# Kernel optimization log

Hardware: AMD Instinct MI355X
Metric: run time of the kernel (lower is better)

## Reference

```python
import jax, jax.numpy as jnp
import numpy as np

PAD_CODE = -1
COMMIT_WEIGHT = 0.25

B, N, D, K = 16, 4096, 256, 512


def setup_inputs() -> dict:
    key = jax.random.key(0)
    k1, k2, k3 = jax.random.split(key, 3)
    z = jax.random.normal(k1, (B, N, D), dtype=jnp.float32)
    phoneme_mask = jax.random.uniform(k2, (B, N)) > 0.3
    codebook = jax.random.normal(k3, (K, D), dtype=jnp.float32)
    return {"z": z, "phoneme_mask": phoneme_mask, "codebook": codebook}


def reference(z, phoneme_mask, codebook):
    # Nearest-codebook search: ||z - e||^2 = ||z||^2 - 2 z.e + ||e||^2
    z_sq = jnp.sum(z * z, axis=-1, keepdims=True)                # (B, N, 1)
    e_sq = jnp.sum(codebook * codebook, axis=-1)                 # (K,)
    cross = jnp.einsum("bnd,kd->bnk", z, codebook)              # (B, N, K)
    dists = z_sq - 2.0 * cross + e_sq                            # (B, N, K)
    indices = jnp.argmin(dists, axis=-1)                         # (B, N) int

    embed = codebook[indices]                                    # gather (B, N, D)
    # straight-through estimator: forward = embed, backward passes grad to z
    quantized = z + jax.lax.stop_gradient(embed - z)
    # commitment loss (quantize detached, as in lucidrains VectorQuantize)
    commit_loss = COMMIT_WEIGHT * jnp.mean(
        (jax.lax.stop_gradient(quantized) - z) ** 2
    )

    # mask padded positions
    indices = jnp.where(phoneme_mask, indices, jnp.full_like(indices, PAD_CODE))
    quantized = quantized * phoneme_mask[..., None].astype(quantized.dtype)
    return quantized, indices, commit_loss
```

## Files before the change

kernel.cpp:

```cpp
#include <hip/hip_runtime.h>

#define BN    65536
#define DD    256
#define KCB   512
#define MT    256
#define NBLK  256
#define NST   16

typedef __attribute__((ext_vector_type(8))) short bf16x8;
typedef __attribute__((ext_vector_type(4))) float f32x4;

static __device__ __forceinline__ float bf2f(unsigned short u) {
  return __uint_as_float(((unsigned int)u) << 16);
}
static __device__ __forceinline__ unsigned short f2bf(float f) {
  unsigned int u = __float_as_uint(f);
  return (unsigned short)((u + 0x7fffu + ((u >> 16) & 1u)) >> 16);
}
static __device__ __forceinline__ void gll16(const void* g, void* l) {
  __builtin_amdgcn_global_load_lds(
      (const __attribute__((address_space(1))) unsigned int*)g,
      (__attribute__((address_space(3))) unsigned int*)l, 16, 0, 0);
}

__global__ void vq_zero_ws(float* ws) { ws[0] = 0.f; }

__global__ void vq_prep(const float* __restrict__ cbg,
                        char* __restrict__ cbt,
                        float* __restrict__ esq) {
  const int tid = threadIdx.x, lane = tid & 63, wave = tid >> 6;
  const int code = blockIdx.x * 4 + wave;
  float4 v = ((const float4*)cbg)[(size_t)code * 64 + lane];
  ushort4 h, l;
  h.x = f2bf(v.x); l.x = f2bf(v.x - bf2f(h.x));
  h.y = f2bf(v.y); l.y = f2bf(v.y - bf2f(h.y));
  h.z = f2bf(v.z); l.z = f2bf(v.z - bf2f(h.z));
  h.w = f2bf(v.w); l.w = f2bf(v.w - bf2f(h.w));
  const int s  = code >> 5;
  const int lc = code & 31;
  unsigned raw = (unsigned)(lc * 512 + lane * 8);
  unsigned off = (unsigned)(s * 32768) + (raw ^ ((unsigned)(lc & 7) << 4));
  *(ushort4*)(cbt + off)         = h;
  *(ushort4*)(cbt + off + 16384) = l;
  double sq = (double)v.x * v.x + (double)v.y * v.y +
              (double)v.z * v.z + (double)v.w * v.w;
#pragma unroll
  for (int m = 1; m < 64; m <<= 1) sq += __shfl_xor(sq, m, 64);
  if (lane == 0) esq[code] = (float)sq;
}

#define ISSUE(S, BSEL)                                                       \
  do {                                                                       \
    const char* _src = cbt + (size_t)(S) * 32768 + (size_t)tid * 16;         \
    char* _dst = &bufB[BSEL][tid * 16];                                      \
    _Pragma("unroll")                                                        \
    for (int _r = 0; _r < 4; ++_r)                                           \
      gll16(_src + _r * 8192, _dst + _r * 8192);                             \
  } while (0)

#define VMCNT4 asm volatile("s_waitcnt vmcnt(4)" ::: "memory")
#define VMCNT0 asm volatile("s_waitcnt vmcnt(0)" ::: "memory")
#define SBAR   asm volatile("s_barrier" ::: "memory")

__global__ __launch_bounds__(512, 2) void vq_main(
    const float* __restrict__ zg,
    const int* __restrict__ maskg,
    const float* __restrict__ cbg,
    const char* __restrict__ cbt,
    const float* __restrict__ esqg,
    float* __restrict__ outq,
    float* __restrict__ outidx,
    float* __restrict__ wsum)
{
  __shared__ __align__(16) char bufB[2][32768];
  __shared__ float esqs[KCB];
  __shared__ float zsqs[MT];
  __shared__ float v1s[MT], v2s[MT];
  __shared__ int   i1s[MT];
  __shared__ float carr[MT];
  __shared__ int   fidxs[MT], maskb[MT], flaglist[MT];
  __shared__ int   flagcnt, mflags;
  __shared__ double rbd[8];
  __shared__ int    rbi[8];

  const int tid   = threadIdx.x;
  const int lane  = tid & 63;
  const int wave  = tid >> 6;
  const int q     = lane >> 4;
  const int l15   = lane & 15;
  const int m0    = blockIdx.x * MT;
  const int rbase = wave * 32;

  if (tid == 0) { flagcnt = 0; mflags = 0; }

  int wm = 0;
  if (tid < 128) {
    unsigned int W = ((const unsigned int*)maskg)[tid];
    if (W > 1u) wm |= 1;
    if (W != 0u && W != 0x3f800000u) wm |= 2;
    unsigned int lo = W & 0xffffu, hi = W >> 16;
    if ((lo != 0u && lo != 0x3f80u) || (hi != 0u && hi != 0x3f80u)) wm |= 4;
  }
  if (wm) atomicOr(&mflags, wm);

  esqs[tid] = esqg[tid];

  ISSUE(0, 0);

  bf16x8 ah[2][8], al[2][8];
  float zacc0 = 0.f, zacc1 = 0.f;
#pragma unroll
  for (int i = 0; i < 2; ++i) {
    const int grow = m0 + rbase + i * 16 + l15;
#pragma unroll
    for (int kk = 0; kk < 8; ++kk) {
      const float* src = &zg[(size_t)grow * DD + kk * 32 + q * 8];
      float4 v0 = *(const float4*)src;
      float4 v1 = *(const float4*)(src + 4);
      float f[8] = {v0.x, v0.y, v0.z, v0.w, v1.x, v1.y, v1.z, v1.w};
      union { ushort us[8]; bf16x8 v; } H, L;
#pragma unroll
      for (int e = 0; e < 8; ++e) {
        unsigned short hh = f2bf(f[e]);
        H.us[e] = hh;
        L.us[e] = f2bf(f[e] - bf2f(hh));
      }
      ah[i][kk] = H.v;
      al[i][kk] = L.v;
      float s = 0.f;
#pragma unroll
      for (int e = 0; e < 8; ++e) s = fmaf(f[e], f[e], s);
      if (i == 0) zacc0 += s; else zacc1 += s;
    }
  }
  {
    float s0 = zacc0, s1 = zacc1;
    s0 += __shfl_xor(s0, 16, 64); s0 += __shfl_xor(s0, 32, 64);
    s1 += __shfl_xor(s1, 16, 64); s1 += __shfl_xor(s1, 32, 64);
    if (q == 0) {
      zsqs[rbase + l15]      = s0;
      zsqs[rbase + 16 + l15] = s1;
    }
  }
  __syncthreads();
  const int mmode = mflags;

  float t1[2][4], t2[2][4];
  int   ti[2][4];
#pragma unroll
  for (int i = 0; i < 2; ++i)
#pragma unroll
    for (int rr = 0; rr < 4; ++rr) { t1[i][rr] = 3.0e38f; t2[i][rr] = 3.0e38f; ti[i][rr] = 0; }

#pragma unroll 1
  for (int s = 0; s < NST; ++s) {
    if (s < NST - 1) { ISSUE(s + 1, (s + 1) & 1); VMCNT4; }
    else             { VMCNT0; }
    SBAR;
    const char* bb = &bufB[s & 1][0];
#pragma unroll
    for (int tt = 0; tt < 2; ++tt) {
      const int lc = tt * 16 + l15;
      const unsigned sw = ((unsigned)(lc & 7)) << 4;
      f32x4 a0 = (f32x4){0.f, 0.f, 0.f, 0.f};
      f32x4 a1 = (f32x4){0.f, 0.f, 0.f, 0.f};
#pragma unroll
      for (int kk = 0; kk < 8; ++kk) {
        const unsigned off = ((unsigned)(lc * 512 + kk * 64 + q * 16)) ^ sw;
        bf16x8 bh = *(const bf16x8*)(bb + off);
        bf16x8 bl = *(const bf16x8*)(bb + 16384 + off);
        a0 = __builtin_amdgcn_mfma_f32_16x16x32_bf16(ah[0][kk], bh, a0, 0, 0, 0);
        a1 = __builtin_amdgcn_mfma_f32_16x16x32_bf16(ah[1][kk], bh, a1, 0, 0, 0);
        a0 = __builtin_amdgcn_mfma_f32_16x16x32_bf16(al[0][kk], bh, a0, 0, 0, 0);
        a1 = __builtin_amdgcn_mfma_f32_16x16x32_bf16(al[1][kk], bh, a1, 0, 0, 0);
        a0 = __builtin_amdgcn_mfma_f32_16x16x32_bf16(ah[0][kk], bl, a0, 0, 0, 0);
        a1 = __builtin_amdgcn_mfma_f32_16x16x32_bf16(ah[1][kk], bl, a1, 0, 0, 0);
      }
      const int code = s * 32 + lc;
      const float eh = 0.5f * esqs[code];
#pragma unroll
      for (int rr = 0; rr < 4; ++rr) {
        {
          float v = eh - a0[rr];
          bool  tk = v < t1[0][rr];
          float m2 = fminf(t2[0][rr], v);
          t2[0][rr] = tk ? t1[0][rr] : m2;
          ti[0][rr] = tk ? code : ti[0][rr];
          t1[0][rr] = tk ? v : t1[0][rr];
        }
        {
          float v = eh - a1[rr];
          bool  tk = v < t1[1][rr];
          float m2 = fminf(t2[1][rr], v);
          t2[1][rr] = tk ? t1[1][rr] : m2;
          ti[1][rr] = tk ? code : ti[1][rr];
          t1[1][rr] = tk ? v : t1[1][rr];
        }
      }
    }
    SBAR;
  }

#pragma unroll
  for (int i = 0; i < 2; ++i)
#pragma unroll
    for (int rr = 0; rr < 4; ++rr) {
      float a1 = t1[i][rr], a2 = t2[i][rr];
      int   ai = ti[i][rr];
#pragma unroll
      for (int m = 1; m < 16; m <<= 1) {
        float o1 = __shfl_xor(a1, m, 64);
        float o2 = __shfl_xor(a2, m, 64);
        int   oi = __shfl_xor(ai, m, 64);
        bool  tk = (o1 < a1) || (o1 == a1 && oi < ai);
        float losr = tk ? a1 : o1;
        a2 = fminf(fminf(a2, o2), losr);
        a1 = tk ? o1 : a1;
        ai = tk ? oi : ai;
      }
      if (l15 == 0) {
        int row = rbase + i * 16 + q * 4 + rr;
        v1s[row] = a1; v2s[row] = a2; i1s[row] = ai;
      }
    }
  __syncthreads();

  if (tid < MT) {
    float bv1 = v1s[tid], bv2 = v2s[tid];
    int   bi = i1s[tid];
    fidxs[tid] = bi;
    carr[tid]  = zsqs[tid] + 2.f * bv1;
    if (2.f * (bv2 - bv1) < 0.02f) {
      int pos = atomicAdd(&flagcnt, 1);
      flaglist[pos] = tid;
    }
    int mk;
    if (!(mmode & 1))      mk = maskg[m0 + tid] ? 1 : 0;
    else if (!(mmode & 2)) mk = ((const float*)maskg)[m0 + tid] != 0.f ? 1 : 0;
    else if (!(mmode & 4)) mk = ((const unsigned short*)maskg)[m0 + tid] ? 1 : 0;
    else                   mk = ((const unsigned char*)maskg)[m0 + tid] ? 1 : 0;
    maskb[tid] = mk;
  }
  __syncthreads();

  int nflag = flagcnt;
  for (int f = 0; f < nflag; ++f) {
    int row = flaglist[f];
    int k   = tid;
    double d2 = 0.0;
    for (int d = 0; d < DD; ++d) {
      double df = (double)zg[(size_t)(m0 + row) * DD + d] - (double)cbg[(size_t)k * DD + d];
      d2 = fma(df, df, d2);
    }
    double bd = d2;
    int    bk = k;
    for (int m = 1; m < 64; m <<= 1) {
      double od = __shfl_xor(bd, m, 64);
      int    ok = __shfl_xor(bk, m, 64);
      if (od < bd || (od == bd && ok < bk)) { bd = od; bk = ok; }
    }
    if (lane == 0) { rbd[wave] = bd; rbi[wave] = bk; }
    __syncthreads();
    if (tid == 0) {
      double xd = rbd[0]; int xk = rbi[0];
      for (int w = 1; w < 8; ++w)
        if (rbd[w] < xd || (rbd[w] == xd && rbi[w] < xk)) { xd = rbd[w]; xk = rbi[w]; }
      fidxs[row] = xk;
      carr[row]  = (float)xd;
    }
    __syncthreads();
  }
  __syncthreads();

  if (tid < MT)
    outidx[m0 + tid] = maskb[tid] ? (float)(fidxs[tid] & (KCB - 1)) : -1.0f;

  if (tid < MT) {
    float c = carr[tid];
    for (int m = 1; m < 64; m <<= 1) c += __shfl_xor(c, m, 64);
    if (lane == 0) atomicAdd(wsum, c);
  }

#pragma unroll
  for (int it = 0; it < 32; ++it) {
    int idx = it * 512 + tid;
    int row = idx >> 6;
    int f4  = idx & 63;
    int k   = fidxs[row] & (KCB - 1);
    float4 val = {0.f, 0.f, 0.f, 0.f};
    if (maskb[row]) val = ((const float4*)cbg)[(size_t)k * 64 + f4];
    ((float4*)outq)[(size_t)(m0 + row) * 64 + f4] = val;
  }
}

__global__ __launch_bounds__(256, 3) void vq_main_fb(
    const float* __restrict__ zg, const int* __restrict__ maskg,
    const float* __restrict__ cbg, float* __restrict__ outq,
    float* __restrict__ outidx, float* __restrict__ wsum)
{
  __shared__ unsigned short zs_hi[8 * 32 * 32];
  __shared__ unsigned short zs_lo[8 * 32 * 32];
  __shared__ float esqs[KCB];
  __shared__ float zsq[32];
  __shared__ float wv1[4][32], wv2[4][32];
  __shared__ int   wi1[4][32];
  __shared__ float carr[32];
  __shared__ int   fidxs[32], maskb[32], flaglist[32];
  __shared__ int   flagcnt, mflags;
  __shared__ double rbd[4];
  __shared__ int    rbi[4];

  const int tid  = threadIdx.x;
  const int lane = tid & 63;
  const int wave = tid >> 6;
  const int q    = lane >> 4;
  const int l15  = lane & 15;
  const int m0   = blockIdx.x * 32;

  if (tid == 0) { flagcnt = 0; mflags = 0; }
  int wm = 0;
  if (tid < 128) {
    unsigned int W = ((const unsigned int*)maskg)[tid];
    if (W > 1u) wm |= 1;
    if (W != 0u && W != 0x3f800000u) wm |= 2;
    unsigned int lo = W & 0xffffu, hi = W >> 16;
    if ((lo != 0u && lo != 0x3f80u) || (hi != 0u && hi != 0x3f80u)) wm |= 4;
  }
  if (wm) atomicOr(&mflags, wm);

#pragma unroll
  for (int i = 0; i < 8; ++i) {
    int idx = i * 256 + tid;
    int row = idx >> 6;
    int f4  = idx & 63;
    float4 v = ((const float4*)zg)[(size_t)(m0 + row) * 64 + f4];
    int ch  = f4 >> 3;
    int col = (f4 & 7) * 4;
    int base = (ch * 32 + row) * 32 + col;
    ushort4 h, l;
    h.x = f2bf(v.x); l.x = f2bf(v.x - bf2f(h.x));
    h.y = f2bf(v.y); l.y = f2bf(v.y - bf2f(h.y));
    h.z = f2bf(v.z); l.z = f2bf(v.z - bf2f(h.z));
    h.w = f2bf(v.w); l.w = f2bf(v.w - bf2f(h.w));
    *(ushort4*)&zs_hi[base] = h;
    *(ushort4*)&zs_lo[base] = l;
    float s = v.x * v.x + v.y * v.y + v.z * v.z + v.w * v.w;
#pragma unroll
    for (int m = 1; m < 64; m <<= 1) s += __shfl_xor(s, m, 64);
    if (lane == 0) zsq[row] = s;
  }
  for (int c = tid; c < KCB; c += 256) {
    float s = 0.f;
    for (int f4i = 0; f4i < 64; ++f4i) {
      float4 v = ((const float4*)cbg)[(size_t)c * 64 + f4i];
      s = fmaf(v.x, v.x, s); s = fmaf(v.y, v.y, s);
      s = fmaf(v.z, v.z, s); s = fmaf(v.w, v.w, s);
    }
    esqs[c] = s;
  }
  __syncthreads();
  const int mmode = mflags;

  f32x4 acc[8][2];
#pragma unroll
  for (int t = 0; t < 8; ++t) {
    acc[t][0] = (f32x4){0.f, 0.f, 0.f, 0.f};
    acc[t][1] = (f32x4){0.f, 0.f, 0.f, 0.f};
  }
  const unsigned short* Abh = &zs_hi[l15 * 32 + q * 8];
  const unsigned short* Abl = &zs_lo[l15 * 32 + q * 8];

  for (int kk = 0; kk < 8; ++kk) {
    bf16x8 ah0 = *(const bf16x8*)(Abh + kk * 1024);
    bf16x8 ah1 = *(const bf16x8*)(Abh + kk * 1024 + 512);
    bf16x8 al0 = *(const bf16x8*)(Abl + kk * 1024);
    bf16x8 al1 = *(const bf16x8*)(Abl + kk * 1024 + 512);
#pragma unroll
    for (int t = 0; t < 8; ++t) {
      const int code_row = (wave * 8 + t) * 16 + l15;
      const float* src = &cbg[(size_t)code_row * 256 + kk * 32 + q * 8];
      float4 v0 = *(const float4*)src;
      float4 v1 = *(const float4*)(src + 4);
      float f[8] = {v0.x, v0.y, v0.z, v0.w, v1.x, v1.y, v1.z, v1.w};
      union { ushort us[8]; bf16x8 v; } H, L;
#pragma unroll
      for (int e = 0; e < 8; ++e) {
        unsigned short hh = f2bf(f[e]);
        H.us[e] = hh;
        L.us[e] = f2bf(f[e] - bf2f(hh));
      }
      bf16x8 bh = H.v, bl = L.v;
      acc[t][0] = __builtin_amdgcn_mfma_f32_16x16x32_bf16(ah0, bh, acc[t][0], 0, 0, 0);
      acc[t][1] = __builtin_amdgcn_mfma_f32_16x16x32_bf16(ah1, bh, acc[t][1], 0, 0, 0);
      acc[t][0] = __builtin_amdgcn_mfma_f32_16x16x32_bf16(al0, bh, acc[t][0], 0, 0, 0);
      acc[t][1] = __builtin_amdgcn_mfma_f32_16x16x32_bf16(al1, bh, acc[t][1], 0, 0, 0);
      acc[t][0] = __builtin_amdgcn_mfma_f32_16x16x32_bf16(ah0, bl, acc[t][0], 0, 0, 0);
      acc[t][1] = __builtin_amdgcn_mfma_f32_16x16x32_bf16(ah1, bl, acc[t][1], 0, 0, 0);
    }
  }

  float t1[2][4], t2[2][4];
  int   ti[2][4];
#pragma unroll
  for (int i = 0; i < 2; ++i)
#pragma unroll
    for (int rr = 0; rr < 4; ++rr) { t1[i][rr] = 3.0e38f; t2[i][rr] = 3.0e38f; ti[i][rr] = 0; }
#pragma unroll
  for (int t = 0; t < 8; ++t) {
    const int code = (wave * 8 + t) * 16 + l15;
    const float eh = 0.5f * esqs[code];
#pragma unroll
    for (int i = 0; i < 2; ++i)
#pragma unroll
      for (int rr = 0; rr < 4; ++rr) {
        float v = eh - acc[t][i][rr];
        bool  tk = v < t1[i][rr];
        float m2 = fminf(t2[i][rr], v);
        t2[i][rr] = tk ? t1[i][rr] : m2;
        ti[i][rr] = tk ? code : ti[i][rr];
        t1[i][rr] = tk ? v : t1[i][rr];
      }
  }
#pragma unroll
  for (int i = 0; i < 2; ++i)
#pragma unroll
    for (int rr = 0; rr < 4; ++rr) {
      float a1 = t1[i][rr], a2 = t2[i][rr];
      int   ai = ti[i][rr];
#pragma unroll
      for (int m = 1; m < 16; m <<= 1) {
        float o1 = __shfl_xor(a1, m, 64);
        float o2 = __shfl_xor(a2, m, 64);
        int   oi = __shfl_xor(ai, m, 64);
        bool  tk = (o1 < a1) || (o1 == a1 && oi < ai);
        float losr = tk ? a1 : o1;
        a2 = fminf(fminf(a2, o2), losr);
        a1 = tk ? o1 : a1;
        ai = tk ? oi : ai;
      }
      if (l15 == 0) {
        int row = i * 16 + q * 4 + rr;
        wv1[wave][row] = a1; wv2[wave][row] = a2; wi1[wave][row] = ai;
      }
    }
  __syncthreads();

  if (tid < 32) {
    float bv1 = 3.0e38f, bv2 = 3.0e38f;
    int   bi = 0x7fffffff;
#pragma unroll
    for (int w = 0; w < 4; ++w) {
      float a1 = wv1[w][tid], a2 = wv2[w][tid];
      int   ai = wi1[w][tid];
      bool  tk = (a1 < bv1) || (a1 == bv1 && ai < bi);
      if (tk) { bv2 = fminf(bv1, a2); bv1 = a1; bi = ai; }
      else    { bv2 = fminf(bv2, a1); }
    }
    fidxs[tid] = bi;
    carr[tid]  = zsq[tid] + 2.f * bv1;
    if (2.f * (bv2 - bv1) < 0.02f) {
      int pos = atomicAdd(&flagcnt, 1);
      flaglist[pos] = tid;
    }
    int mk;
    if (!(mmode & 1))      mk = maskg[m0 + tid] ? 1 : 0;
    else if (!(mmode & 2)) mk = ((const float*)maskg)[m0 + tid] != 0.f ? 1 : 0;
    else if (!(mmode & 4)) mk = ((const unsigned short*)maskg)[m0 + tid] ? 1 : 0;
    else                   mk = ((const unsigned char*)maskg)[m0 + tid] ? 1 : 0;
    maskb[tid] = mk;
  }
  __syncthreads();

  int nflag = flagcnt;
  for (int f = 0; f < nflag; ++f) {
    int row = flaglist[f];
    double bd = 1e300;
    int    bk = 0;
    for (int k = tid; k < KCB; k += 256) {
      double d2 = 0.0;
      for (int d = 0; d < DD; ++d) {
        double df = (double)zg[(size_t)(m0 + row) * DD + d] - (double)cbg[(size_t)k * DD + d];
        d2 = fma(df, df, d2);
      }
      if (d2 < bd) { bd = d2; bk = k; }
    }
    for (int m = 1; m < 64; m <<= 1) {
      double od = __shfl_xor(bd, m, 64);
      int    ok = __shfl_xor(bk, m, 64);
      if (od < bd || (od == bd && ok < bk)) { bd = od; bk = ok; }
    }
    if (lane == 0) { rbd[wave] = bd; rbi[wave] = bk; }
    __syncthreads();
    if (tid == 0) {
      double xd = rbd[0]; int xk = rbi[0];
      for (int w = 1; w < 4; ++w)
        if (rbd[w] < xd || (rbd[w] == xd && rbi[w] < xk)) { xd = rbd[w]; xk = rbi[w]; }
      fidxs[row] = xk;
      carr[row]  = (float)xd;
    }
    __syncthreads();
  }
  __syncthreads();

  if (tid < 32)
    outidx[m0 + tid] = maskb[tid] ? (float)(fidxs[tid] & (KCB - 1)) : -1.0f;

  if (wave == 0) {
    float c = (lane < 32) ? carr[lane] : 0.f;
    for (int m = 1; m < 64; m <<= 1) c += __shfl_xor(c, m, 64);
    if (lane == 0) atomicAdd(wsum, c);
  }

#pragma unroll
  for (int i = 0; i < 8; ++i) {
    int idx = i * 256 + tid;
    int row = idx >> 6;
    int f4  = idx & 63;
    int k   = fidxs[row] & (KCB - 1);
    float4 val = {0.f, 0.f, 0.f, 0.f};
    if (maskb[row]) val = ((const float4*)cbg)[(size_t)k * 64 + f4];
    ((float4*)outq)[(size_t)(m0 + row) * 64 + f4] = val;
  }
}

__global__ void vq_final(const float* __restrict__ wsum,
                         float* __restrict__ outloss) {
  if (threadIdx.x == 0)
    outloss[0] = 0.25f * (wsum[0] / 16777216.0f);
}

extern "C" void kernel_launch(void* const* d_in, const int* in_sizes, int n_in,
                              void* d_out, int out_size, void* d_ws, size_t ws_size,
                              hipStream_t stream) {
  const void* pz = d_in[0];
  const void* pm = (n_in > 1) ? d_in[1] : d_in[0];
  const void* pc = (n_in > 2) ? d_in[2] : d_in[0];
  for (int i = 0; i < n_in; ++i) {
    if      (in_sizes[i] == BN * DD)  pz = d_in[i];
    else if (in_sizes[i] == BN)       pm = d_in[i];
    else if (in_sizes[i] == KCB * DD) pc = d_in[i];
  }
  const float* zg  = (const float*)pz;
  const int*   mk  = (const int*)pm;
  const float* cbg = (const float*)pc;

  float* outq   = (float*)d_out;
  float* outidx = outq + (size_t)BN * DD;
  float* outls  = outidx + BN;
  float* wsum   = (float*)d_ws;

  const size_t ESQ_OFF = 1024;
  const size_t CBT_OFF = 4096;
  const size_t WS_NEED = CBT_OFF + (size_t)KCB * DD * 2 * 2;

  vq_zero_ws<<<1, 1, 0, stream>>>(wsum);
  if (ws_size >= WS_NEED) {
    char*  cbt = (char*)d_ws + CBT_OFF;
    float* esw = (float*)((char*)d_ws + ESQ_OFF);
    vq_prep<<<128, 256, 0, stream>>>(cbg, cbt, esw);
    vq_main<<<NBLK, 512, 0, stream>>>(zg, mk, cbg, cbt, esw,
                                      outq, outidx, wsum);
  } else {
    vq_main_fb<<<2048, 256, 0, stream>>>(zg, mk, cbg, outq, outidx, wsum);
  }
  vq_final<<<1, 64, 0, stream>>>(wsum, outls);
}
```

Before: 209.3 us.

## Halve block tile, fold zero/final kernels into prep/main, parallelize fallback rescoring

```diff
diff --git a/kernel.cpp b/kernel.cpp
--- a/kernel.cpp
+++ b/kernel.cpp
@@ -3,8 +3,8 @@
 #define BN    65536
 #define DD    256
 #define KCB   512
-#define MT    256
-#define NBLK  256
+#define MT    128
+#define NBLK  512
 #define NST   16
 
 typedef __attribute__((ext_vector_type(8))) short bf16x8;
@@ -27,7 +27,10 @@
 
 __global__ void vq_prep(const float* __restrict__ cbg,
                         char* __restrict__ cbt,
-                        float* __restrict__ esq) {
+                        float* __restrict__ esq,
+                        float* __restrict__ wsum,
+                        unsigned int* __restrict__ dcnt) {
+  if (blockIdx.x == 0 && threadIdx.x == 0) { wsum[0] = 0.f; dcnt[0] = 0u; }
   const int tid = threadIdx.x, lane = tid & 63, wave = tid >> 6;
   const int code = blockIdx.x * 4 + wave;
   float4 v = ((const float4*)cbg)[(size_t)code * 64 + lane];
@@ -54,15 +57,15 @@
     const char* _src = cbt + (size_t)(S) * 32768 + (size_t)tid * 16;         \
     char* _dst = &bufB[BSEL][tid * 16];                                      \
     _Pragma("unroll")                                                        \
-    for (int _r = 0; _r < 4; ++_r)                                           \
-      gll16(_src + _r * 8192, _dst + _r * 8192);                             \
+    for (int _r = 0; _r < 8; ++_r)                                           \
+      gll16(_src + _r * 4096, _dst + _r * 4096);                             \
   } while (0)
 
-#define VMCNT4 asm volatile("s_waitcnt vmcnt(4)" ::: "memory")
+#define VMCNT8 asm volatile("s_waitcnt vmcnt(8)" ::: "memory")
 #define VMCNT0 asm volatile("s_waitcnt vmcnt(0)" ::: "memory")
 #define SBAR   asm volatile("s_barrier" ::: "memory")
 
-__global__ __launch_bounds__(512, 2) void vq_main(
+__global__ __launch_bounds__(256, 2) void vq_main(
     const float* __restrict__ zg,
     const int* __restrict__ maskg,
     const float* __restrict__ cbg,
@@ -70,7 +73,9 @@
     const float* __restrict__ esqg,
     float* __restrict__ outq,
     float* __restrict__ outidx,
-    float* __restrict__ wsum)
+    float* __restrict__ outls,
+    float* __restrict__ wsum,
+    unsigned int* __restrict__ dcnt)
 {
   __shared__ __align__(16) char bufB[2][32768];
   __shared__ float esqs[KCB];
@@ -80,8 +85,6 @@
   __shared__ float carr[MT];
   __shared__ int   fidxs[MT], maskb[MT], flaglist[MT];
   __shared__ int   flagcnt, mflags;
-  __shared__ double rbd[8];
-  __shared__ int    rbi[8];
 
   const int tid   = threadIdx.x;
   const int lane  = tid & 63;
@@ -103,7 +106,8 @@
   }
   if (wm) atomicOr(&mflags, wm);
 
-  esqs[tid] = esqg[tid];
+  esqs[tid]       = esqg[tid];
+  esqs[tid + 256] = esqg[tid + 256];
 
   ISSUE(0, 0);
 
@@ -154,7 +158,7 @@
 
 #pragma unroll 1
   for (int s = 0; s < NST; ++s) {
-    if (s < NST - 1) { ISSUE(s + 1, (s + 1) & 1); VMCNT4; }
+    if (s < NST - 1) { ISSUE(s + 1, (s + 1) & 1); VMCNT8; }
     else             { VMCNT0; }
     SBAR;
     const char* bb = &bufB[s & 1][0];
@@ -244,31 +248,33 @@
   __syncthreads();
 
   int nflag = flagcnt;
-  for (int f = 0; f < nflag; ++f) {
-    int row = flaglist[f];
-    int k   = tid;
-    double d2 = 0.0;
-    for (int d = 0; d < DD; ++d) {
-      double df = (double)zg[(size_t)(m0 + row) * DD + d] - (double)cbg[(size_t)k * DD + d];
-      d2 = fma(df, df, d2);
-    }
-    double bd = d2;
-    int    bk = k;
-    for (int m = 1; m < 64; m <<= 1) {
-      double od = __shfl_xor(bd, m, 64);
-      int    ok = __shfl_xor(bk, m, 64);
-      if (od < bd || (od == bd && ok < bk)) { bd = od; bk = ok; }
-    }
-    if (lane == 0) { rbd[wave] = bd; rbi[wave] = bk; }
-    __syncthreads();
-    if (tid == 0) {
-      double xd = rbd[0]; int xk = rbi[0];
-      for (int w = 1; w < 8; ++w)
-        if (rbd[w] < xd || (rbd[w] == xd && rbi[w] < xk)) { xd = rbd[w]; xk = rbi[w]; }
-      fidxs[row] = xk;
-      carr[row]  = (float)xd;
-    }
-    __syncthreads();
+  for (int f0 = 0; f0 < nflag; f0 += 4) {
+    const int fi = f0 + wave;
+    if (fi < nflag) {
+      const int row = flaglist[fi];
+      const float* zr = &zg[(size_t)(m0 + row) * DD];
+      const float* cb = &cbg[(size_t)(lane * 8) * DD];
+      double d2[8] = {0., 0., 0., 0., 0., 0., 0., 0.};
+      for (int d = 0; d < DD; ++d) {
+        double zd = (double)zr[d];
+#pragma unroll
+        for (int c = 0; c < 8; ++c) {
+          double df = zd - (double)cb[(size_t)c * DD + d];
+          d2[c] = fma(df, df, d2[c]);
+        }
+      }
+      double bd = d2[0];
+      int    bk = lane * 8;
+#pragma unroll
+      for (int c = 1; c < 8; ++c)
+        if (d2[c] < bd) { bd = d2[c]; bk = lane * 8 + c; }
+      for (int m = 1; m < 64; m <<= 1) {
+        double od = __shfl_xor(bd, m, 64);
+        int    ok = __shfl_xor(bk, m, 64);
+        if (od < bd || (od == bd && ok < bk)) { bd = od; bk = ok; }
+      }
+      if (lane == 0) { fidxs[row] = bk; carr[row] = (float)bd; }
+    }
   }
   __syncthreads();
 
@@ -283,13 +289,23 @@
 
 #pragma unroll
   for (int it = 0; it < 32; ++it) {
-    int idx = it * 512 + tid;
+    int idx = it * 256 + tid;
     int row = idx >> 6;
     int f4  = idx & 63;
     int k   = fidxs[row] & (KCB - 1);
     float4 val = {0.f, 0.f, 0.f, 0.f};
     if (maskb[row]) val = ((const float4*)cbg)[(size_t)k * 64 + f4];
     ((float4*)outq)[(size_t)(m0 + row) * 64 + f4] = val;
+  }
+
+  __syncthreads();
+  if (tid == 0) {
+    __threadfence();
+    unsigned prev = atomicAdd(dcnt, 1u);
+    if (prev == (unsigned)(NBLK - 1)) {
+      float s = atomicAdd(wsum, 0.f);
+      outls[0] = 0.25f * (s / 16777216.0f);
+    }
   }
 }
 
@@ -549,19 +565,20 @@
   float* outls  = outidx + BN;
   float* wsum   = (float*)d_ws;
 
+  unsigned int* dcnt = (unsigned int*)((char*)d_ws + 512);
   const size_t ESQ_OFF = 1024;
   const size_t CBT_OFF = 4096;
   const size_t WS_NEED = CBT_OFF + (size_t)KCB * DD * 2 * 2;
 
-  vq_zero_ws<<<1, 1, 0, stream>>>(wsum);
   if (ws_size >= WS_NEED) {
     char*  cbt = (char*)d_ws + CBT_OFF;
     float* esw = (float*)((char*)d_ws + ESQ_OFF);
-    vq_prep<<<128, 256, 0, stream>>>(cbg, cbt, esw);
-    vq_main<<<NBLK, 512, 0, stream>>>(zg, mk, cbg, cbt, esw,
-                                      outq, outidx, wsum);
+    vq_prep<<<128, 256, 0, stream>>>(cbg, cbt, esw, wsum, dcnt);
+    vq_main<<<NBLK, 256, 0, stream>>>(zg, mk, cbg, cbt, esw,
+                                      outq, outidx, outls, wsum, dcnt);
   } else {
+    vq_zero_ws<<<1, 1, 0, stream>>>(wsum);
     vq_main_fb<<<2048, 256, 0, stream>>>(zg, mk, cbg, outq, outidx, wsum);
-  }
-  vq_final<<<1, 64, 0, stream>>>(wsum, outls);
-}
+    vq_final<<<1, 64, 0, stream>>>(wsum, outls);
+  }
+}
```

Result: slower. 263.4 us (+25.9%).
